# Optimization experiments

Measured on AMD Instinct MI355X. Metric: run time of the kernel, lower is better.

## Reference

```python
import jax, jax.numpy as jnp
import numpy as np

CLIP_VAL = 32

def setup_inputs() -> dict:
    key = jax.random.key(0)
    ks = jax.random.split(key, 8)
    B, T, D_MODEL, H, DK = 4, 1024, 1024, 16, 64
    s = 0.02  # small init scale, glorot-like magnitude
    return {
        "query": jax.random.normal(ks[0], (B, T, D_MODEL), jnp.float32),
        "value": jax.random.normal(ks[1], (B, T, D_MODEL), jnp.float32),
        "W_Q": jax.random.normal(ks[2], (H, D_MODEL, DK), jnp.float32) * s,
        "W_K": jax.random.normal(ks[3], (H, D_MODEL, DK), jnp.float32) * s,
        "W_V": jax.random.normal(ks[4], (H, D_MODEL, DK), jnp.float32) * s,
        "W_O": jax.random.normal(ks[5], (H, DK, D_MODEL), jnp.float32) * s,
        "emb_Q": jax.random.normal(ks[6], (2 * CLIP_VAL + 1, DK), jnp.float32) * s,
        "emb_S": jax.random.normal(ks[7], (2 * CLIP_VAL + 1, DK), jnp.float32) * s,
    }

def reference(query, value, W_Q, W_K, W_V, W_O, emb_Q, emb_S):
    # query/value: (B, T, D_Model); per-head weights: (H, D_Model, Dk)
    T = query.shape[1]
    Dk = W_Q.shape[-1]
    sqrt_D = jnp.sqrt(jnp.asarray(Dk, query.dtype))

    # relative position index matrix: (T, T) ints in [0, 2*clip]
    tau = jnp.arange(T)
    rel = (jnp.clip(tau[None, :] - tau[:, None], -CLIP_VAL, CLIP_VAL) + CLIP_VAL)
    eQ = emb_Q[rel]  # (T, T, Dk) relative key embedding
    eS = emb_S[rel]  # (T, T, Dv) relative value embedding

    qW = jnp.einsum('btm,hmd->bhtd', query, W_Q)  # (B,H,T,Dk)
    kW = jnp.einsum('btm,hmd->bhtd', value, W_K)
    vW = jnp.einsum('btm,hmd->bhtd', value, W_V)

    # content scores + relative-query bias, both scaled by 1/sqrt(Dk)
    scores = (jnp.einsum('bhtd,bhsd->bhts', qW, kW)
              + jnp.einsum('bhtd,tsd->bhts', qW, eQ)) / sqrt_D
    p = jax.nn.softmax(scores, axis=-1)  # (B,H,T,T)

    # value combination + relative-value term
    heads = (jnp.einsum('bhts,bhsd->bhtd', p, vW)
             + jnp.einsum('bhts,tsd->bhtd', p, eS))

    # per-head output projection then sum over heads
    out = jnp.einsum('bhtd,hdm->btm', heads, W_O)  # (B,T,D_Model)
    return out
```

## Files before the change

### kernel.cpp

```cpp
#include <hip/hip_runtime.h>
#include <math.h>


typedef _Float16 f16;
typedef f16 half8 __attribute__((ext_vector_type(8)));
typedef f16 half4v __attribute__((ext_vector_type(4)));
typedef float f32x4 __attribute__((ext_vector_type(4)));
typedef float f32x16 __attribute__((ext_vector_type(16)));

__global__ __launch_bounds__(256) void prep(
    const float* __restrict__ q, const float* __restrict__ v,
    const float* __restrict__ W0, const float* __restrict__ W1,
    const float* __restrict__ W2, const float* __restrict__ WO,
    f16* __restrict__ q16, f16* __restrict__ Wt16, f16* __restrict__ WOt16) {
    __shared__ float tile[64][65];
    const int bx = blockIdx.x;
    const int t = threadIdx.x;
    if (bx < 8192) {
        int i = (bx * 256 + t) * 4;
        const float* s = (i < 4194304) ? (q + i) : (v + (i - 4194304));
        float4 x = *(const float4*)s;
        half4v h = {(f16)x.x, (f16)x.y, (f16)x.z, (f16)x.w};
        *(half4v*)&q16[i] = h;
        return;
    }
    const int c = t & 63, r4 = t >> 6;
    const int n = t >> 2, kc = (t & 3) * 16;
    if (bx < 8960) {
        const int idx = bx - 8192;
        const int z = idx >> 4, k0 = (idx & 15) * 64;
        const float* src = ((z < 16) ? W0 : (z < 32) ? W1 : W2) + (size_t)(z & 15) * 65536;
        f16* out = Wt16 + (size_t)z * 65536;
#pragma unroll
        for (int p = 0; p < 16; ++p)
            tile[r4 + p * 4][c] = src[(size_t)(k0 + r4 + p * 4) * 64 + c];
        __syncthreads();
        f16 buf[16];
#pragma unroll
        for (int i = 0; i < 16; ++i) buf[i] = (f16)tile[kc + i][n];
        *(half8*)&out[(size_t)n * 1024 + k0 + kc] = *(half8*)&buf[0];
        *(half8*)&out[(size_t)n * 1024 + k0 + kc + 8] = *(half8*)&buf[8];
        return;
    }
    {
        const int idx = bx - 8960;
        const int k0 = (idx & 15) * 64, n0 = (idx >> 4) * 64;
#pragma unroll
        for (int p = 0; p < 16; ++p)
            tile[r4 + p * 4][c] = WO[(size_t)(k0 + r4 + p * 4) * 1024 + n0 + c];
        __syncthreads();
        f16 buf[16];
#pragma unroll
        for (int i = 0; i < 16; ++i) buf[i] = (f16)tile[kc + i][n];
        *(half8*)&WOt16[(size_t)(n0 + n) * 1024 + k0 + kc] = *(half8*)&buf[0];
        *(half8*)&WOt16[(size_t)(n0 + n) * 1024 + k0 + kc + 8] = *(half8*)&buf[8];
    }
}

template <int MODE, int NT, bool DBUF>
__global__ __launch_bounds__(256) void mfma_gemm(
    const f16* __restrict__ Aq, const f16* __restrict__ Av,
    const f16* __restrict__ Bt, float* __restrict__ C,
    f16* __restrict__ oQ, f16* __restrict__ oK, f16* __restrict__ oVt) {
    constexpr int K = 1024;
    constexpr int NI = NT / 32;
    constexpr int LDSZ = (128 + NT) * 64;
    constexpr int NX = (MODE == 0) ? 24 : 16;
    const int f = blockIdx.x;
    const int cpx = gridDim.x >> 3;
    const int swz = (f & 7) * cpx + (f >> 3);
    const int n0 = (swz % NX) * NT;
    const int m0 = (swz / NX) * 128;
    const f16* Abase = (MODE == 0) ? ((n0 < 1024) ? Aq : Av) : Aq;

    __shared__ f16 lds[LDSZ * (DBUF ? 2 : 1)];

    const int tid = threadIdx.x;
    const int l = tid & 63, wv = tid >> 6;
    const int rseg = l >> 3;
    const int g = (l & 7) ^ rseg;
    const bool isA = (wv < 2);
    const int rowBase = isA ? (wv & 1) * 64 : (wv & 1) * (NT / 2);
    const int nLoads = isA ? 8 : (NT / 16);
    const f16* gSrc = isA ? (Abase + (size_t)m0 * K) : (Bt + (size_t)n0 * K);
    const f16* gLane = gSrc + (size_t)(rowBase + rseg) * K + g * 8;
    const int ldsRow0 = (isA ? 0 : 128) + rowBase;

    const int fr = l & 15, fq = l >> 4, sw = fr & 7;
    const int mi2 = wv & 1, ni2 = wv >> 1;
    int aOff[NI], bOff[4];
#pragma unroll
    for (int i = 0; i < 4; ++i) bOff[i] = (mi2 * 64 + i * 16 + fr) * 128;
#pragma unroll
    for (int i = 0; i < NI; ++i)
        aOff[i] = (128 + ni2 * (NT / 2) + i * 16 + fr) * 128;

    f32x4 acc[4][NI];
#pragma unroll
    for (int i = 0; i < 4; ++i)
#pragma unroll
        for (int j = 0; j < NI; ++j) acc[i][j] = {0.f, 0.f, 0.f, 0.f};

    auto issue = [&](int k0, int buf) {
        f16* dst = lds + (buf ? LDSZ : 0);
#pragma unroll 8
        for (int i = 0; i < nLoads; ++i) {
            const f16* src = gLane + (size_t)i * 8 * K + k0;
            __builtin_amdgcn_global_load_lds(
                (const __attribute__((address_space(1))) unsigned int*)src,
                (__attribute__((address_space(3))) unsigned int*)
                    &dst[(ldsRow0 + i * 8) * 64], 16, 0, 0);
        }
    };

    if (DBUF) issue(0, 0);
    int it = 0;
    for (int k0 = 0; k0 < K; k0 += 64, ++it) {
        if (!DBUF) issue(k0, 0);
        __syncthreads();
        if (DBUF && k0 + 64 < K) issue(k0 + 64, (it + 1) & 1);
        const char* lp = (const char*)lds + (DBUF ? (it & 1) * (LDSZ * 2) : 0);
#pragma unroll
        for (int kk = 0; kk < 2; ++kk) {
            const int glq = kk * 4 + fq;
            const int sgl = (glq ^ sw) * 16;
            half8 aF[NI], bF[4];
#pragma unroll
            for (int i = 0; i < NI; ++i)
                aF[i] = *(const half8*)(lp + aOff[i] + sgl);
#pragma unroll
            for (int i = 0; i < 4; ++i)
                bF[i] = *(const half8*)(lp + bOff[i] + sgl);
#pragma unroll
            for (int mi = 0; mi < 4; ++mi)
#pragma unroll
                for (int ni = 0; ni < NI; ++ni)
                    acc[mi][ni] = __builtin_amdgcn_mfma_f32_16x16x32_f16(
                        aF[ni], bF[mi], acc[mi][ni], 0, 0, 0);
        }
        if (!DBUF) __syncthreads();
    }
#pragma unroll
    for (int mi = 0; mi < 4; ++mi) {
        const int m = m0 + mi2 * 64 + mi * 16 + fr;
#pragma unroll
        for (int ni = 0; ni < NI; ++ni) {
            const int n = n0 + ni2 * (NT / 2) + ni * 16 + 4 * fq;
            if (MODE == 1) {
                *(f32x4*)(C + (size_t)m * 1024 + n) = acc[mi][ni];
            } else {
                const int w = n >> 10, h = (n >> 6) & 15, d = n & 63;
                const int b = m >> 10, t = m & 1023;
                const size_t bh = (size_t)(b * 16 + h);
                f32x4 a = acc[mi][ni];
                if (w == 0) {
                    half4v hv = {(f16)(a[0] * 0.125f), (f16)(a[1] * 0.125f),
                                 (f16)(a[2] * 0.125f), (f16)(a[3] * 0.125f)};
                    *(half4v*)&oQ[bh * 65536 + (size_t)t * 64 + d] = hv;
                } else if (w == 1) {
                    half4v hv = {(f16)a[0], (f16)a[1], (f16)a[2], (f16)a[3]};
                    *(half4v*)&oK[bh * 65536 + (size_t)t * 64 + d] = hv;
                } else {
#pragma unroll
                    for (int r = 0; r < 4; ++r)
                        oVt[bh * 65536 + (size_t)(d + r) * 1024 + t] = (f16)a[r];
                }
            }
        }
    }
}

__global__ __launch_bounds__(256, 2) void attn_kernel(
    const f16* __restrict__ q16a, const f16* __restrict__ k16,
    const f16* __restrict__ vt16, const float* __restrict__ embQ,
    const float* __restrict__ embS, f16* __restrict__ heads16) {
    const int bh = blockIdx.x;
    const int t0 = blockIdx.y * 128;
    const f16* qg = q16a + (size_t)bh * 65536;
    const f16* kg = k16 + (size_t)bh * 65536;
    const f16* vg = vt16 + (size_t)bh * 65536;

    __shared__ f16 Kt[2][4096];
    __shared__ f16 Vt[2][4096];
    __shared__ f16 qEl[66 * 136];
    __shared__ f16 band[128 * 72];
    __shared__ float e64s[64];

    const int tid = threadIdx.x;
    const int wv = tid >> 6, lane = tid & 63;
    const int tl32 = lane & 31, h = lane >> 5;
    const int tl = wv * 32 + tl32;
    const int tg = t0 + tl;

    auto stageKV = [&](int j0, int buf) {
#pragma unroll
        for (int i = 0; i < 2; ++i) {
            const int rt = wv * 16 + i * 8 + (lane >> 3);
            const int g = (lane & 7) ^ (rt & 7);
            __builtin_amdgcn_global_load_lds(
                (const __attribute__((address_space(1))) unsigned int*)
                    (kg + (size_t)(j0 + rt) * 64 + g * 8),
                (__attribute__((address_space(3))) unsigned int*)
                    &Kt[buf][(wv * 16 + i * 8) * 64], 16, 0, 0);
            __builtin_amdgcn_global_load_lds(
                (const __attribute__((address_space(1))) unsigned int*)
                    (vg + (size_t)rt * 1024 + j0 + g * 8),
                (__attribute__((address_space(3))) unsigned int*)
                    &Vt[buf][(wv * 16 + i * 8) * 64], 16, 0, 0);
        }
    };

    half8 qf[4];
#pragma unroll
    for (int ks = 0; ks < 4; ++ks)
        qf[ks] = *(const half8*)&qg[(size_t)tg * 64 + (2 * ks + h) * 8];
    stageKV(0, 0);

    f16* embQs = band;
    for (int idx = tid; idx < 768; idx += 256) {
        const int row = idx >> 3, p = idx & 7, g = p ^ (row & 7);
        half8 hv;
        if (row < 65) {
            const float* s = embQ + row * 64 + g * 8;
#pragma unroll
            for (int j = 0; j < 8; ++j) hv[j] = (f16)s[j];
        } else {
#pragma unroll
            for (int j = 0; j < 8; ++j) hv[j] = (f16)0.f;
        }
        *(half8*)&embQs[row * 64 + p * 8] = hv;
    }
    __syncthreads();
    {
        f32x16 qacc[3];
#pragma unroll
        for (int mt = 0; mt < 3; ++mt)
#pragma unroll
            for (int r = 0; r < 16; ++r) qacc[mt][r] = 0.f;
#pragma unroll
        for (int ks = 0; ks < 4; ++ks)
#pragma unroll
            for (int mt = 0; mt < 3; ++mt) {
                const int row = tl32 + 32 * mt;
                const int p = (2 * ks + h) ^ (row & 7);
                half8 ef = *(const half8*)&embQs[row * 64 + p * 8];
                qacc[mt] = __builtin_amdgcn_mfma_f32_32x32x16_f16(
                    ef, qf[ks], qacc[mt], 0, 0, 0);
            }
        __syncthreads();
#pragma unroll
        for (int mt = 0; mt < 3; ++mt)
#pragma unroll
            for (int r = 0; r < 16; ++r) {
                const int rr = (r & 3) + 8 * (r >> 2) + 4 * h + 32 * mt;
                if (rr < 65) qEl[rr * 136 + tl] = (f16)qacc[mt][r];
            }
    }
    for (int idx = tid; idx < 1152; idx += 256) {
        half8 hv;
#pragma unroll
        for (int j = 0; j < 8; ++j) hv[j] = (f16)(-1.0e4f);
        *(half8*)&band[idx * 8] = hv;
    }
    if (tid < 64) e64s[tid] = embS[64 * 64 + tid];
    __syncthreads();
    const float qE0 = (float)qEl[tl];
    const float qE64 = (float)qEl[64 * 136 + tl];

    float rs = 0.f, rsL = 0.f;
    f32x16 oacc[2];
#pragma unroll
    for (int dt = 0; dt < 2; ++dt)
#pragma unroll
        for (int r = 0; r < 16; ++r) oacc[dt][r] = 0.f;

    for (int jt = 0; jt < 16; ++jt) {
        const int j0 = jt * 64;
        __syncthreads();
        if (jt < 15) stageKV(j0 + 64, (jt + 1) & 1);
        const f16* Ktc = Kt[jt & 1];
        const f16* Vtc = Vt[jt & 1];
        f32x16 sacc[2];
#pragma unroll
        for (int mt = 0; mt < 2; ++mt)
#pragma unroll
            for (int r = 0; r < 16; ++r) sacc[mt][r] = 0.f;
#pragma unroll
        for (int ks = 0; ks < 4; ++ks)
#pragma unroll
            for (int mt = 0; mt < 2; ++mt) {
                const int row = tl32 + 32 * mt;
                const int p = (2 * ks + h) ^ (row & 7);
                half8 kf = *(const half8*)&Ktc[row * 64 + p * 8];
                sacc[mt] = __builtin_amdgcn_mfma_f32_32x32x16_f16(
                    kf, qf[ks], sacc[mt], 0, 0, 0);
            }
        const int dj = j0 - t0;
        if (dj <= -128 || dj >= 192) {
            const float bias = (dj < 0) ? qE0 : qE64;
            float ts = 0.f;
#pragma unroll
            for (int mt = 0; mt < 2; ++mt)
#pragma unroll
                for (int r = 0; r < 16; ++r) {
                    float pe = __expf(sacc[mt][r] + bias);
                    sacc[mt][r] = pe; ts += pe;
                }
            rs += ts;
            if (dj < 0) rsL += ts;
        } else {
#pragma unroll
            for (int mt = 0; mt < 2; ++mt)
#pragma unroll
                for (int r = 0; r < 16; ++r) {
                    const int sg = j0 + 32 * mt + (r & 3) + 8 * (r >> 2) + 4 * h;
                    const int ds = sg - tg;
                    const int dc = ds < -32 ? -32 : (ds > 32 ? 32 : ds);
                    float v = sacc[mt][r] + (float)qEl[(dc + 32) * 136 + tl];
                    if (ds >= -31 && ds <= 31) band[tl * 72 + ds + 31] = (f16)v;
                    float pe = __expf(v);
                    sacc[mt][r] = pe; rs += pe;
                    if (ds <= -32) rsL += pe;
                }
        }
#pragma unroll
        for (int ks = 0; ks < 4; ++ks) {
            const int mtile = ks >> 1, rb = (ks & 1) * 8;
            float ex[4];
#pragma unroll
            for (int c = 0; c < 4; ++c) {
                float send = (h == 0) ? sacc[mtile][rb + 4 + c]
                                      : sacc[mtile][rb + c];
                ex[c] = __shfl_xor(send, 32);
            }
            half8 pf;
#pragma unroll
            for (int j = 0; j < 4; ++j)
                pf[j] = (f16)((h == 0) ? sacc[mtile][rb + j] : ex[j]);
#pragma unroll
            for (int j = 0; j < 4; ++j)
                pf[4 + j] = (f16)((h == 0) ? ex[j] : sacc[mtile][rb + 4 + j]);
#pragma unroll
            for (int dt = 0; dt < 2; ++dt) {
                const int row = tl32 + 32 * dt;
                const int p = (2 * ks + h) ^ (row & 7);
                half8 vf = *(const half8*)&Vtc[row * 64 + p * 8];
                oacc[dt] = __builtin_amdgcn_mfma_f32_32x32x16_f16(
                    vf, pf, oacc[dt], 0, 0, 0);
            }
        }
    }
    rs += __shfl_xor(rs, 32);
    rsL += __shfl_xor(rsL, 32);
    float sumBand = 0.f;
#pragma unroll
    for (int c = 0; c < 4; ++c) {
        const int kb = 32 * h + 8 * c;
        half8 bv = *(const half8*)&band[tl * 72 + kb];
        half8 ev;
#pragma unroll
        for (int j = 0; j < 8; ++j) {
            const int k = kb + j;
            float v;
            if (k == 63) v = rsL;
            else { v = __expf((float)bv[j]); sumBand += v; }
            ev[j] = (f16)v;
        }
        *(half8*)&band[tl * 72 + kb] = ev;
    }
    sumBand += __shfl_xor(sumBand, 32);
    const float sumR = rs - rsL - sumBand;
    for (int idx = tid; idx < 512; idx += 256) {
        const int d = idx >> 3, p = idx & 7, g = p ^ (d & 7);
        half8 hv;
#pragma unroll
        for (int j = 0; j < 8; ++j) {
            const int k = g * 8 + j;
            hv[j] = (f16)embS[((k == 63) ? 0 : (k + 1)) * 64 + d];
        }
        *(half8*)&Kt[0][d * 64 + p * 8] = hv;
    }
    __syncthreads();
#pragma unroll
    for (int ks = 0; ks < 4; ++ks) {
        half8 pf = *(const half8*)&band[tl * 72 + 16 * ks + 8 * h];
#pragma unroll
        for (int dt = 0; dt < 2; ++dt) {
            const int row = tl32 + 32 * dt;
            const int p = (2 * ks + h) ^ (row & 7);
            half8 ef = *(const half8*)&Kt[0][row * 64 + p * 8];
            oacc[dt] = __builtin_amdgcn_mfma_f32_32x32x16_f16(
                ef, pf, oacc[dt], 0, 0, 0);
        }
    }
    __syncthreads();
    const float inv = 1.0f / rs;
#pragma unroll
    for (int dt = 0; dt < 2; ++dt)
#pragma unroll
        for (int r = 0; r < 16; ++r) {
            const int d = (r & 3) + 8 * (r >> 2) + 4 * h + 32 * dt;
            band[tl * 72 + d] = (f16)((oacc[dt][r] + sumR * e64s[d]) * inv);
        }
    __syncthreads();
    const int b = bh >> 4, hh = bh & 15;
    const int row = tid >> 1, cb = (tid & 1) * 32;
    f16* dst = heads16 + ((size_t)(b * 1024 + t0 + row) * 1024) + hh * 64 + cb;
#pragma unroll
    for (int c = 0; c < 4; ++c)
        *(half8*)&dst[c * 8] = *(const half8*)&band[row * 72 + cb + c * 8];
}

extern "C" void kernel_launch(void* const* d_in, const int* in_sizes, int n_in,
                              void* d_out, int out_size, void* d_ws, size_t ws_size,
                              hipStream_t stream) {
    const float* query = (const float*)d_in[0];
    const float* value = (const float*)d_in[1];
    const float* WQ   = (const float*)d_in[2];
    const float* WK   = (const float*)d_in[3];
    const float* WV   = (const float*)d_in[4];
    const float* WO   = (const float*)d_in[5];
    const float* embQ = (const float*)d_in[6];
    const float* embS = (const float*)d_in[7];
    float* out = (float*)d_out;

    f16* w0    = (f16*)d_ws;
    f16* q16   = w0;
    f16* v16   = w0 + 4194304;
    f16* Wt16  = w0 + 8388608;
    f16* WOt16 = w0 + 11534336;
    f16* q16a  = w0 + 12582912;
    f16* k16   = w0 + 16777216;
    f16* vt16  = w0 + 20971520;
    f16* h16   = w0 + 25165824;

    prep<<<9216, 256, 0, stream>>>(query, value, WQ, WK, WV, WO,
                                   q16, Wt16, WOt16);
    mfma_gemm<0, 128, true><<<768, 256, 0, stream>>>(
        q16, v16, Wt16, nullptr, q16a, k16, vt16);
    attn_kernel<<<dim3(64, 8), 256, 0, stream>>>(q16a, k16, vt16, embQ, embS, h16);
    mfma_gemm<1, 64, true><<<512, 256, 0, stream>>>(
        h16, h16, WOt16, out, nullptr, nullptr, nullptr);
}
```

Before: 206.9 us.

## Transpose V tiles through LDS, fold log2e into Q scale, add MFMA priority hints

The projection GEMM now writes the transposed V output by staging the tile in shared memory and storing contiguous half8 rows. Before, each thread issued scattered 2-byte stores. The Q scale now includes log2(e), so the attention kernel can use exp2f in place of __expf. s_setprio hints are placed around the MFMA blocks so that waves issuing matrix ops get scheduling priority. The V path adds extra LDS traffic and barriers, and it relies on the qE bias terms also being in log2 units for the result to stay correct.

```diff
diff --git a/kernel.cpp b/kernel.cpp
--- a/kernel.cpp
+++ b/kernel.cpp
@@ -140,6 +140,33 @@
         }
         if (!DBUF) __syncthreads();
     }
+    if (MODE == 0 && n0 >= 2048) {
+        __syncthreads();
+        f16* Tr = lds;
+#pragma unroll
+        for (int mi = 0; mi < 4; ++mi) {
+            const int ml = mi2 * 64 + mi * 16 + fr;
+#pragma unroll
+            for (int ni = 0; ni < NI; ++ni) {
+                const int nl = ni2 * (NT / 2) + ni * 16 + 4 * fq;
+                f32x4 a = acc[mi][ni];
+#pragma unroll
+                for (int r = 0; r < 4; ++r)
+                    Tr[(nl + r) * 136 + ml] = (f16)a[r];
+            }
+        }
+        __syncthreads();
+        const int b = m0 >> 10, t0m = m0 & 1023;
+        const int hh = (n0 >> 6) & 15;
+        const int row = tid >> 1, cb = (tid & 1) * 64;
+        const size_t bh = (size_t)(b * 16 + hh + (row >> 6));
+        const int d = row & 63;
+        f16* dst = oVt + bh * 65536 + (size_t)d * 1024 + t0m + cb;
+#pragma unroll
+        for (int c = 0; c < 8; ++c)
+            *(half8*)&dst[c * 8] = *(const half8*)&Tr[row * 136 + cb + c * 8];
+        return;
+    }
 #pragma unroll
     for (int mi = 0; mi < 4; ++mi) {
         const int m = m0 + mi2 * 64 + mi * 16 + fr;
@@ -154,16 +181,13 @@
                 const size_t bh = (size_t)(b * 16 + h);
                 f32x4 a = acc[mi][ni];
                 if (w == 0) {
-                    half4v hv = {(f16)(a[0] * 0.125f), (f16)(a[1] * 0.125f),
-                                 (f16)(a[2] * 0.125f), (f16)(a[3] * 0.125f)};
+                    const float sc = 0.18033688f;
+                    half4v hv = {(f16)(a[0] * sc), (f16)(a[1] * sc),
+                                 (f16)(a[2] * sc), (f16)(a[3] * sc)};
                     *(half4v*)&oQ[bh * 65536 + (size_t)t * 64 + d] = hv;
-                } else if (w == 1) {
+                } else {
                     half4v hv = {(f16)a[0], (f16)a[1], (f16)a[2], (f16)a[3]};
                     *(half4v*)&oK[bh * 65536 + (size_t)t * 64 + d] = hv;
-                } else {
-#pragma unroll
-                    for (int r = 0; r < 4; ++r)
-                        oVt[bh * 65536 + (size_t)(d + r) * 1024 + t] = (f16)a[r];
                 }
             }
         }
@@ -285,6 +309,7 @@
         for (int mt = 0; mt < 2; ++mt)
 #pragma unroll
             for (int r = 0; r < 16; ++r) sacc[mt][r] = 0.f;
+        __builtin_amdgcn_s_setprio(1);
 #pragma unroll
         for (int ks = 0; ks < 4; ++ks)
 #pragma unroll
@@ -295,6 +320,7 @@
                 sacc[mt] = __builtin_amdgcn_mfma_f32_32x32x16_f16(
                     kf, qf[ks], sacc[mt], 0, 0, 0);
             }
+        __builtin_amdgcn_s_setprio(0);
         const int dj = j0 - t0;
         if (dj <= -128 || dj >= 192) {
             const float bias = (dj < 0) ? qE0 : qE64;
@@ -303,7 +329,7 @@
             for (int mt = 0; mt < 2; ++mt)
 #pragma unroll
                 for (int r = 0; r < 16; ++r) {
-                    float pe = __expf(sacc[mt][r] + bias);
+                    float pe = exp2f(sacc[mt][r] + bias);
                     sacc[mt][r] = pe; ts += pe;
                 }
             rs += ts;
@@ -318,7 +344,7 @@
                     const int dc = ds < -32 ? -32 : (ds > 32 ? 32 : ds);
                     float v = sacc[mt][r] + (float)qEl[(dc + 32) * 136 + tl];
                     if (ds >= -31 && ds <= 31) band[tl * 72 + ds + 31] = (f16)v;
-                    float pe = __expf(v);
+                    float pe = exp2f(v);
                     sacc[mt][r] = pe; rs += pe;
                     if (ds <= -32) rsL += pe;
                 }
@@ -340,6 +366,7 @@
 #pragma unroll
             for (int j = 0; j < 4; ++j)
                 pf[4 + j] = (f16)((h == 0) ? ex[j] : sacc[mtile][rb + 4 + j]);
+            __builtin_amdgcn_s_setprio(1);
 #pragma unroll
             for (int dt = 0; dt < 2; ++dt) {
                 const int row = tl32 + 32 * dt;
@@ -348,6 +375,7 @@
                 oacc[dt] = __builtin_amdgcn_mfma_f32_32x32x16_f16(
                     vf, pf, oacc[dt], 0, 0, 0);
             }
+            __builtin_amdgcn_s_setprio(0);
         }
     }
     rs += __shfl_xor(rs, 32);
@@ -363,7 +391,7 @@
             const int k = kb + j;
             float v;
             if (k == 63) v = rsL;
-            else { v = __expf((float)bv[j]); sumBand += v; }
+            else { v = exp2f((float)bv[j]); sumBand += v; }
             ev[j] = (f16)v;
         }
         *(half8*)&band[tl * 72 + kb] = ev;
```

Result: faster. 201.7 us (-2.5%).
